# Optimization experiments

Hardware: AMD Instinct MI355X
Metric: run time of the kernel (lower is better)

## Reference

```python
import jax, jax.numpy as jnp
import numpy as np

BH, BW = 64, 64            # base model input (block) size
STRIDE = 16                # block // 4, per WindowObjectDetector.predict
N_CLASSES = 10
THRESH = 0.7


def _extract_patches(x, bh, bw, stride):
    # x: [1, H, W, 3] -> [R, C, bh, bw, 3], VALID padding (tf.image.extract_patches)
    H, W = x.shape[1], x.shape[2]
    R = (H - bh) // stride + 1
    C = (W - bw) // stride + 1
    r = (jnp.arange(R) * stride)[:, None] + jnp.arange(bh)   # [R, bh]
    c = (jnp.arange(C) * stride)[:, None] + jnp.arange(bw)   # [C, bw]
    p = x[0][r]                 # [R, bh, W, 3]
    p = p[:, :, c]              # [R, bh, C, bw, 3]
    return jnp.transpose(p, (0, 2, 1, 3, 4))  # [R, C, bh, bw, 3]


def _connected_components(mask):
    # mask: bool [K, R, C]; 4-connectivity min-label propagation.
    K, R, C = mask.shape
    BIG = jnp.int32(R * C + 2)
    seed = (jnp.arange(R * C, dtype=jnp.int32).reshape(R, C) + 1)[None]  # [1,R,C]
    lbl0 = jnp.where(mask, seed, 0)

    def prop(l):
        xm = jnp.where(mask, l, BIG)
        n = xm
        n = jnp.minimum(n, jnp.pad(xm, ((0, 0), (1, 0), (0, 0)), constant_values=R * C + 2)[:, :R, :])
        n = jnp.minimum(n, jnp.pad(xm, ((0, 0), (0, 1), (0, 0)), constant_values=R * C + 2)[:, 1:, :])
        n = jnp.minimum(n, jnp.pad(xm, ((0, 0), (0, 0), (1, 0)), constant_values=R * C + 2)[:, :, :C])
        n = jnp.minimum(n, jnp.pad(xm, ((0, 0), (0, 0), (0, 1)), constant_values=R * C + 2)[:, :, 1:])
        return jnp.where(mask, n, 0)

    def cond(carry):
        prev, cur = carry
        return jnp.any(prev != cur)

    def body(carry):
        _, cur = carry
        return cur, prop(cur)

    _, lbl = jax.lax.while_loop(cond, body, (lbl0, prop(lbl0)))
    return lbl  # [K, R, C] int32, 0 = background


def _boxes_from_labels(labels):
    # labels: [K, R, C] -> padded boxes [K, R*C+1, 4] (rowmin-1, colmin-1, rowmax+1, colmax+1)
    K, R, C = labels.shape
    S = R * C + 1
    rr = jnp.repeat(jnp.arange(R, dtype=jnp.int32), C)  # [R*C]
    cc = jnp.tile(jnp.arange(C, dtype=jnp.int32), R)
    flat = labels.reshape(K, R * C)

    def per_class(lbl_k):
        rmin = jax.ops.segment_min(rr, lbl_k, num_segments=S)
        rmax = jax.ops.segment_max(rr, lbl_k, num_segments=S)
        cmin = jax.ops.segment_min(cc, lbl_k, num_segments=S)
        cmax = jax.ops.segment_max(cc, lbl_k, num_segments=S)
        cnt = jax.ops.segment_sum(jnp.ones_like(lbl_k), lbl_k, num_segments=S)
        valid = (cnt > 0) & (jnp.arange(S) > 0)
        box = jnp.stack([rmin - 1, cmin - 1, rmax + 1, cmax + 1], axis=-1)
        box = jnp.where(valid[:, None], box, -1)
        return box, valid

    return jax.vmap(per_class)(flat)


def setup_inputs() -> dict:
    key = jax.random.key(0)
    k1, k2, k3 = jax.random.split(key, 3)
    inputs = jax.random.uniform(k1, (1, 1024, 1024, 3), dtype=jnp.float32)
    W = jax.random.normal(k2, (BH * BW * 3, N_CLASSES), dtype=jnp.float32) * 0.02
    b = jax.random.normal(k3, (N_CLASSES,), dtype=jnp.float32)
    return {"inputs": inputs, "W": W, "b": b}


def reference(inputs, W, b):
    # Windowing: extract 64x64 patches with stride 16 (image divisible by 64 -> no resize)
    patches = _extract_patches(inputs, BH, BW, STRIDE)          # [R, C, 64, 64, 3]
    R, C = patches.shape[0], patches.shape[1]
    flat = patches.reshape(R * C, BH * BW * 3)
    logits = flat @ W + b                                        # base model
    prob = jax.nn.softmax(logits, axis=1).reshape(R, C, N_CLASSES)
    mask = prob > THRESH                                         # [R, C, K]
    # tf transposes before/after connected_components (4-connectivity is symmetric)
    labels = _connected_components(jnp.transpose(mask, (2, 0, 1)))  # [K, R, C]
    labels = jnp.transpose(labels, (1, 2, 0))                    # [R, C, K]
    boxes, valid = _boxes_from_labels(jnp.transpose(labels, (2, 0, 1)))
    return prob, labels, boxes, valid
```

## Files before the change

kernel.cpp:

```cpp
#include <hip/hip_runtime.h>
#include <math.h>

#define RG 61
#define CG 61
#define NP 3721
#define NSEG 3722
#define NCLS 10
#define THRESHV 0.7f
#define BIGI 0x3FFFFFFF

#define NKQ 16
#define NBLK (RG*NKQ)
#define PAD 54

__global__ __launch_bounds__(256, 4) void wod_logits_part(
    const float* __restrict__ img,
    const float* __restrict__ W,
    float* __restrict__ part)
{
    __shared__ float simg[64 * PAD];
    __shared__ float sw[1920];
    __shared__ float scr[1280];

    const int tid = threadIdx.x;
    const int o  = (blockIdx.x & 7) * 122 + (blockIdx.x >> 3);
    const int r  = o >> 4;
    const int kq = o & 15;

    const int wv = tid >> 6, lane = tid & 63;
    const int g  = lane >> 3, qd = lane & 7;
    const int h  = wv & 1,  kh = wv >> 1;
    const int cb = h * 32 + qd * 4;

    int cbase[4];
    #pragma unroll
    for (int t = 0; t < 4; ++t) {
        const int c = cb + t;
        cbase[t] = (c > 60 ? 60 : c) * PAD;
    }

    float acc[4][NCLS];
    #pragma unroll
    for (int t = 0; t < 4; ++t)
        #pragma unroll
        for (int k = 0; k < NCLS; ++k) acc[t][k] = 0.f;

    for (int m = 0; m < 4; ++m) {
        if (m) __syncthreads();
        const int wr = 4 * kq + m;

        const float* wsrc = W + wr * 1920;
        for (int v = tid; v < 480; v += 256)
            *(float4*)(sw + v * 4) = *(const float4*)(wsrc + v * 4);

        const float* isrc = img + (size_t)(16 * r + wr) * 3072;
        for (int v = tid; v < 768; v += 256) {
            const float4 x4 = *(const float4*)(isrc + v * 4);
            const int p0 = v * 4;
            const int ch = p0 / 48;
            float* d = simg + ch * PAD + (p0 - ch * 48);
            d[0] = x4.x; d[1] = x4.y; d[2] = x4.z; d[3] = x4.w;
        }
        __syncthreads();

        #pragma unroll 2
        for (int s = 0; s < 6; ++s) {
            const int pr = kh * 48 + s * 8 + g;
            const float* wp = sw + pr * 20;
            const float4 A0 = *(const float4*)(wp);
            const float4 A1 = *(const float4*)(wp + 4);
            const float4 A2 = *(const float4*)(wp + 8);
            const float4 A3 = *(const float4*)(wp + 12);
            const float4 A4 = *(const float4*)(wp + 16);
            const int q0 = pr * 2;
            const int cq = q0 / 48;
            const float* xb = simg + cq * PAD + (q0 - cq * 48);
            float2 x[4];
            #pragma unroll
            for (int t = 0; t < 4; ++t)
                x[t] = *(const float2*)(xb + cbase[t]);
            const float w0[NCLS] = {A0.x,A0.y,A0.z,A0.w,A1.x,A1.y,A1.z,A1.w,A2.x,A2.y};
            const float w1[NCLS] = {A2.z,A2.w,A3.x,A3.y,A3.z,A3.w,A4.x,A4.y,A4.z,A4.w};
            #pragma unroll
            for (int t = 0; t < 4; ++t)
                #pragma unroll
                for (int k = 0; k < NCLS; ++k) {
                    acc[t][k] = fmaf(x[t].x, w0[k], acc[t][k]);
                    acc[t][k] = fmaf(x[t].y, w1[k], acc[t][k]);
                }
        }
    }

    #pragma unroll
    for (int t = 0; t < 4; ++t)
        #pragma unroll
        for (int k = 0; k < NCLS; ++k) {
            float v = acc[t][k];
            v += __shfl_down(v, 8);
            v += __shfl_down(v, 16);
            v += __shfl_down(v, 32);
            acc[t][k] = v;
        }
    if (g == 0) {
        #pragma unroll
        for (int t = 0; t < 4; ++t)
            #pragma unroll
            for (int k = 0; k < NCLS; ++k)
                scr[wv * 320 + qd * 40 + t * 10 + k] = acc[t][k];
    }
    __syncthreads();
    for (int o2 = tid; o2 < 640; o2 += 256) {
        const int c = o2 / 10, k = o2 - c * 10;
        const int h2 = c >> 5, q2 = (c >> 2) & 7, t2 = c & 3;
        const int idx = q2 * 40 + t2 * 10 + k;
        part[o * 640 + o2] = scr[h2 * 320 + idx] + scr[(h2 + 2) * 320 + idx];
    }
}

__global__ __launch_bounds__(256) void wod_reduce(
    const float* __restrict__ part,
    const float* __restrict__ bias,
    float* __restrict__ out_prob,
    int* __restrict__ mask)
{
    const int cell = blockIdx.x * 256 + threadIdx.x;
    if (cell >= NP) return;
    const int r = cell / CG;
    const int c = cell - r * CG;

    float lg[NCLS];
    #pragma unroll
    for (int k = 0; k < NCLS; ++k) lg[k] = bias[k];
    const float* pb = part + (size_t)r * 16 * 640 + c * 10;
    #pragma unroll
    for (int kq = 0; kq < 16; ++kq)
        #pragma unroll
        for (int k = 0; k < NCLS; ++k) lg[k] += pb[kq * 640 + k];

    float m = -1e30f;
    #pragma unroll
    for (int k = 0; k < NCLS; ++k) m = fmaxf(m, lg[k]);
    float ex[NCLS], sm = 0.f;
    #pragma unroll
    for (int k = 0; k < NCLS; ++k) { ex[k] = expf(lg[k] - m); sm += ex[k]; }
    const float inv = 1.f / sm;
    const int base = cell * NCLS;
    #pragma unroll
    for (int k = 0; k < NCLS; ++k) {
        const float pr = ex[k] * inv;
        out_prob[base + k] = pr;
        mask[k * NP + cell] = (pr > THRESHV) ? 1 : 0;
    }
}

__global__ __launch_bounds__(256) void wod_cc(
    const int* __restrict__ mask,
    float* __restrict__ out_lbl,
    float* __restrict__ out_box,
    float* __restrict__ out_valid)
{
    const int k = blockIdx.x;
    const int tid = threadIdx.x;
    __shared__ int lbl[NP];
    __shared__ int ext0[NSEG], ext1[NSEG];
    __shared__ int changed;

    const int* mk = mask + k * NP;
    for (int idx = tid; idx < NP; idx += 256)
        lbl[idx] = mk[idx] ? (idx + 1) : 0;
    if (tid == 0) changed = 0;
    __syncthreads();

    for (;;) {
        for (int idx = tid; idx < NP; idx += 256) {
            int v = lbl[idx];
            if (v) {
                const int rr = idx / CG;
                const int cc = idx - rr * CG;
                int best = v;
                if (rr > 0)      { int n = lbl[idx - CG]; if (n && n < best) best = n; }
                if (rr < RG - 1) { int n = lbl[idx + CG]; if (n && n < best) best = n; }
                if (cc > 0)      { int n = lbl[idx - 1];  if (n && n < best) best = n; }
                if (cc < CG - 1) { int n = lbl[idx + 1];  if (n && n < best) best = n; }
                if (best < v) { lbl[idx] = best; changed = 1; }
            }
        }
        __syncthreads();
        const bool stop = (changed == 0);
        __syncthreads();
        if (stop) break;
        if (tid == 0) changed = 0;
        __syncthreads();
    }

    for (int idx = tid; idx < NP; idx += 256)
        out_lbl[idx * NCLS + k] = (float)lbl[idx];

    float* boxk = out_box + k * NSEG * 4;
    float* valk = out_valid + k * NSEG;

    for (int s2 = tid; s2 < NSEG; s2 += 256) { ext0[s2] = BIGI; ext1[s2] = BIGI; }
    __syncthreads();
    for (int idx = tid; idx < NP; idx += 256) {
        const int v = lbl[idx];
        if (v) {
            const int rr = idx / CG, cc = idx - rr * CG;
            atomicMin(&ext0[v], rr);
            atomicMin(&ext1[v], cc);
        }
    }
    __syncthreads();
    for (int s2 = tid; s2 < NSEG; s2 += 256) {
        const bool valid = (s2 > 0) && (ext0[s2] != BIGI);
        boxk[s2 * 4 + 0] = valid ? (float)(ext0[s2] - 1) : -1.f;
        boxk[s2 * 4 + 1] = valid ? (float)(ext1[s2] - 1) : -1.f;
        valk[s2] = valid ? 1.f : 0.f;
    }
    __syncthreads();

    for (int s2 = tid; s2 < NSEG; s2 += 256) { ext0[s2] = -1; ext1[s2] = -1; }
    __syncthreads();
    for (int idx = tid; idx < NP; idx += 256) {
        const int v = lbl[idx];
        if (v) {
            const int rr = idx / CG, cc = idx - rr * CG;
            atomicMax(&ext0[v], rr);
            atomicMax(&ext1[v], cc);
        }
    }
    __syncthreads();
    for (int s2 = tid; s2 < NSEG; s2 += 256) {
        const bool valid = (s2 > 0) && (ext0[s2] >= 0);
        boxk[s2 * 4 + 2] = valid ? (float)(ext0[s2] + 1) : -1.f;
        boxk[s2 * 4 + 3] = valid ? (float)(ext1[s2] + 1) : -1.f;
    }
}

extern "C" void kernel_launch(void* const* d_in, const int* in_sizes, int n_in,
                              void* d_out, int out_size, void* d_ws, size_t ws_size,
                              hipStream_t stream) {
    (void)in_sizes; (void)n_in; (void)out_size; (void)ws_size;
    const float* img = (const float*)d_in[0];
    const float* W   = (const float*)d_in[1];
    const float* b   = (const float*)d_in[2];

    float* out       = (float*)d_out;
    float* out_prob  = out;
    float* out_lbl   = out + 37210;
    float* out_box   = out + 74420;
    float* out_valid = out + 223300;

    int*   mask = (int*)d_ws;
    float* part = (float*)((int*)d_ws + NCLS * NP);

    hipLaunchKernelGGL(wod_logits_part, dim3(NBLK), dim3(256), 0, stream,
                       img, W, part);
    hipLaunchKernelGGL(wod_reduce, dim3((NP + 255) / 256), dim3(256), 0, stream,
                       part, b, out_prob, mask);
    hipLaunchKernelGGL(wod_cc, dim3(NCLS), dim3(256), 0, stream,
                       mask, out_lbl, out_box, out_valid);
}
```

Before: 47.17 us.

## Give each wave one kernel row and move the reduction to per-row blocks

The logits kernel now loads all four image rows into shared memory once. Each wave takes one weight row, and each lane computes one output column. Weights are read straight from global memory instead of being staged in shared memory. This removes the cross-lane shuffle reduction, the scratch combine and three block barriers, but it writes 64 partial rows per output row instead of 16. The reduce kernel now runs one block per output row, sums the 64 partials into shared memory and then does the softmax. The new layout adds partial-sum traffic and gives up the 4-column register reuse of each weight load.

```diff
diff --git a/kernel.cpp b/kernel.cpp
--- a/kernel.cpp
+++ b/kernel.cpp
@@ -11,109 +11,76 @@
 
 #define NKQ 16
 #define NBLK (RG*NKQ)
-#define PAD 54
-
-__global__ __launch_bounds__(256, 4) void wod_logits_part(
+#define CHS 50
+#define ROWF (64*CHS)
+#define PROW 610
+
+__global__ __launch_bounds__(256, 3) void wod_logits_part(
     const float* __restrict__ img,
     const float* __restrict__ W,
     float* __restrict__ part)
 {
-    __shared__ float simg[64 * PAD];
-    __shared__ float sw[1920];
-    __shared__ float scr[1280];
+    __shared__ float simg[4 * ROWF];
 
     const int tid = threadIdx.x;
     const int o  = (blockIdx.x & 7) * 122 + (blockIdx.x >> 3);
     const int r  = o >> 4;
     const int kq = o & 15;
-
-    const int wv = tid >> 6, lane = tid & 63;
-    const int g  = lane >> 3, qd = lane & 7;
-    const int h  = wv & 1,  kh = wv >> 1;
-    const int cb = h * 32 + qd * 4;
-
-    int cbase[4];
+    const int R0 = 16 * r + 4 * kq;
+
+    for (int u = tid; u < 3072; u += 256) {
+        const int row = u / 768;
+        const int v   = u - row * 768;
+        const int p0  = v * 4;
+        const float4 x4 = *(const float4*)(img + (size_t)(R0 + row) * 3072 + p0);
+        const int ch = p0 / 48;
+        const int q  = p0 - ch * 48;
+        float* d = simg + row * ROWF + ch * CHS + q;
+        *(float2*)d       = make_float2(x4.x, x4.y);
+        *(float2*)(d + 2) = make_float2(x4.z, x4.w);
+    }
+    __syncthreads();
+
+    const int wv = __builtin_amdgcn_readfirstlane(tid >> 6);
+    const int c  = tid & 63;
+    const int cx = c > 60 ? 60 : c;
+    const int wr = 4 * kq + wv;
+
+    const float* wbase = W + wr * 1920;
+    const float* srow  = simg + wv * ROWF + cx * CHS;
+
+    float acc[NCLS];
     #pragma unroll
-    for (int t = 0; t < 4; ++t) {
-        const int c = cb + t;
-        cbase[t] = (c > 60 ? 60 : c) * PAD;
-    }
-
-    float acc[4][NCLS];
-    #pragma unroll
-    for (int t = 0; t < 4; ++t)
-        #pragma unroll
-        for (int k = 0; k < NCLS; ++k) acc[t][k] = 0.f;
-
-    for (int m = 0; m < 4; ++m) {
-        if (m) __syncthreads();
-        const int wr = 4 * kq + m;
-
-        const float* wsrc = W + wr * 1920;
-        for (int v = tid; v < 480; v += 256)
-            *(float4*)(sw + v * 4) = *(const float4*)(wsrc + v * 4);
-
-        const float* isrc = img + (size_t)(16 * r + wr) * 3072;
-        for (int v = tid; v < 768; v += 256) {
-            const float4 x4 = *(const float4*)(isrc + v * 4);
-            const int p0 = v * 4;
-            const int ch = p0 / 48;
-            float* d = simg + ch * PAD + (p0 - ch * 48);
-            d[0] = x4.x; d[1] = x4.y; d[2] = x4.z; d[3] = x4.w;
-        }
-        __syncthreads();
-
-        #pragma unroll 2
-        for (int s = 0; s < 6; ++s) {
-            const int pr = kh * 48 + s * 8 + g;
-            const float* wp = sw + pr * 20;
+    for (int k = 0; k < NCLS; ++k) acc[k] = 0.f;
+
+    for (int q = 0; q < 24; ++q) {
+        #pragma unroll
+        for (int j = 0; j < 4; ++j) {
+            const int rem = 8 * q + 2 * j;
+            const int chq = rem / 48;
+            const int uq  = chq * CHS + (rem - 48 * chq);
+            const float2 x = *(const float2*)(srow + uq);
+            const float* wp = wbase + rem * 10;
             const float4 A0 = *(const float4*)(wp);
             const float4 A1 = *(const float4*)(wp + 4);
             const float4 A2 = *(const float4*)(wp + 8);
             const float4 A3 = *(const float4*)(wp + 12);
             const float4 A4 = *(const float4*)(wp + 16);
-            const int q0 = pr * 2;
-            const int cq = q0 / 48;
-            const float* xb = simg + cq * PAD + (q0 - cq * 48);
-            float2 x[4];
-            #pragma unroll
-            for (int t = 0; t < 4; ++t)
-                x[t] = *(const float2*)(xb + cbase[t]);
             const float w0[NCLS] = {A0.x,A0.y,A0.z,A0.w,A1.x,A1.y,A1.z,A1.w,A2.x,A2.y};
             const float w1[NCLS] = {A2.z,A2.w,A3.x,A3.y,A3.z,A3.w,A4.x,A4.y,A4.z,A4.w};
             #pragma unroll
-            for (int t = 0; t < 4; ++t)
-                #pragma unroll
-                for (int k = 0; k < NCLS; ++k) {
-                    acc[t][k] = fmaf(x[t].x, w0[k], acc[t][k]);
-                    acc[t][k] = fmaf(x[t].y, w1[k], acc[t][k]);
-                }
-        }
-    }
-
-    #pragma unroll
-    for (int t = 0; t < 4; ++t)
-        #pragma unroll
-        for (int k = 0; k < NCLS; ++k) {
-            float v = acc[t][k];
-            v += __shfl_down(v, 8);
-            v += __shfl_down(v, 16);
-            v += __shfl_down(v, 32);
-            acc[t][k] = v;
-        }
-    if (g == 0) {
-        #pragma unroll
-        for (int t = 0; t < 4; ++t)
-            #pragma unroll
-            for (int k = 0; k < NCLS; ++k)
-                scr[wv * 320 + qd * 40 + t * 10 + k] = acc[t][k];
-    }
-    __syncthreads();
-    for (int o2 = tid; o2 < 640; o2 += 256) {
-        const int c = o2 / 10, k = o2 - c * 10;
-        const int h2 = c >> 5, q2 = (c >> 2) & 7, t2 = c & 3;
-        const int idx = q2 * 40 + t2 * 10 + k;
-        part[o * 640 + o2] = scr[h2 * 320 + idx] + scr[(h2 + 2) * 320 + idx];
+            for (int k = 0; k < NCLS; ++k) {
+                acc[k] = fmaf(x.x, w0[k], acc[k]);
+                acc[k] = fmaf(x.y, w1[k], acc[k]);
+            }
+        }
+    }
+
+    if (c < 61) {
+        float* pr = part + (size_t)(r * 64 + wr) * PROW + c * 10;
+        #pragma unroll
+        for (int k = 0; k < NCLS; k += 2)
+            *(float2*)(pr + k) = make_float2(acc[k], acc[k + 1]);
     }
 }
 
@@ -123,33 +90,38 @@
     float* __restrict__ out_prob,
     int* __restrict__ mask)
 {
-    const int cell = blockIdx.x * 256 + threadIdx.x;
-    if (cell >= NP) return;
-    const int r = cell / CG;
-    const int c = cell - r * CG;
-
-    float lg[NCLS];
-    #pragma unroll
-    for (int k = 0; k < NCLS; ++k) lg[k] = bias[k];
-    const float* pb = part + (size_t)r * 16 * 640 + c * 10;
-    #pragma unroll
-    for (int kq = 0; kq < 16; ++kq)
-        #pragma unroll
-        for (int k = 0; k < NCLS; ++k) lg[k] += pb[kq * 640 + k];
-
-    float m = -1e30f;
-    #pragma unroll
-    for (int k = 0; k < NCLS; ++k) m = fmaxf(m, lg[k]);
-    float ex[NCLS], sm = 0.f;
-    #pragma unroll
-    for (int k = 0; k < NCLS; ++k) { ex[k] = expf(lg[k] - m); sm += ex[k]; }
-    const float inv = 1.f / sm;
-    const int base = cell * NCLS;
-    #pragma unroll
-    for (int k = 0; k < NCLS; ++k) {
-        const float pr = ex[k] * inv;
-        out_prob[base + k] = pr;
-        mask[k * NP + cell] = (pr > THRESHV) ? 1 : 0;
+    __shared__ float lg[PROW];
+    const int r   = blockIdx.x;
+    const int tid = threadIdx.x;
+    const float* pb = part + (size_t)r * 64 * PROW;
+
+    for (int t = tid; t < PROW; t += 256) {
+        float s = bias[t - (t / 10) * 10];
+        const float* p = pb + t;
+        #pragma unroll 8
+        for (int wr = 0; wr < 64; ++wr) s += p[wr * PROW];
+        lg[t] = s;
+    }
+    __syncthreads();
+
+    for (int c = tid; c < CG; c += 256) {
+        float l[NCLS];
+        #pragma unroll
+        for (int k = 0; k < NCLS; ++k) l[k] = lg[c * 10 + k];
+        float m = -1e30f;
+        #pragma unroll
+        for (int k = 0; k < NCLS; ++k) m = fmaxf(m, l[k]);
+        float ex[NCLS], sm = 0.f;
+        #pragma unroll
+        for (int k = 0; k < NCLS; ++k) { ex[k] = expf(l[k] - m); sm += ex[k]; }
+        const float inv = 1.f / sm;
+        const int cell = r * CG + c;
+        #pragma unroll
+        for (int k = 0; k < NCLS; ++k) {
+            const float pr = ex[k] * inv;
+            out_prob[cell * 10 + k] = pr;
+            mask[k * NP + cell] = (pr > THRESHV) ? 1 : 0;
+        }
     }
 }
 
@@ -255,7 +227,7 @@
 
     hipLaunchKernelGGL(wod_logits_part, dim3(NBLK), dim3(256), 0, stream,
                        img, W, part);
-    hipLaunchKernelGGL(wod_reduce, dim3((NP + 255) / 256), dim3(256), 0, stream,
+    hipLaunchKernelGGL(wod_reduce, dim3(RG), dim3(256), 0, stream,
                        part, b, out_prob, mask);
     hipLaunchKernelGGL(wod_cc, dim3(NCLS), dim3(256), 0, stream,
                        mask, out_lbl, out_box, out_valid);
```

Measured after the change: 54.30 us. 1.15x slower.
